# Optimization experiments

Measured on AMD Instinct MI355X. Metric: run time of the kernel, lower is better.

Reference implementation:

```python
import jax, jax.numpy as jnp
import numpy as np

HIDDEN = 128; HEADS = 8; HD = HIDDEN // HEADS; NRBF = 50; NLAYERS = 6
CUT = 5.0; MAXZ = 100
N = 5000; E = 100000


def cosine_cutoff(d):
    # cutoff_lower = 0: 0.5*(cos(pi*d/cut)+1) * (d < cut)
    return 0.5 * (jnp.cos(d * (jnp.pi / CUT)) + 1.0) * (d < CUT)


def expnorm_rbf(d, means, betas):
    # ExpNormalSmearing with cutoff_lower=0, alpha = 5/cutoff
    alpha = 5.0 / CUT
    return cosine_cutoff(d)[:, None] * jnp.exp(-betas * (jnp.exp(-alpha * d)[:, None] - means) ** 2)


def layernorm(x, w, b):
    m = x.mean(-1, keepdims=True)
    v = ((x - m) ** 2).mean(-1, keepdims=True)
    return (x - m) / jnp.sqrt(v + 1e-5) * w + b


def setup_inputs():
    key = jax.random.key(0)
    ks = jax.random.split(key, 16)
    start = float(np.exp(-CUT))

    def lin(k, fi, fo):
        return jax.random.normal(k, (fi, fo), jnp.float32) / np.sqrt(fi)

    def lin_l(k, fi, fo):
        return jax.random.normal(k, (NLAYERS, fi, fo), jnp.float32) / np.sqrt(fi)

    return {
        "z": jax.random.randint(ks[0], (N,), 0, MAXZ),
        "edge_index": jax.random.randint(ks[1], (2, E), 0, N),
        "edge_vec": jax.random.normal(ks[2], (E, 3), jnp.float32) * 1.7,
        "emb": jax.random.normal(ks[3], (MAXZ, HIDDEN), jnp.float32),
        "means": jnp.linspace(start, 1.0, NRBF, dtype=jnp.float32),
        "betas": jnp.full((NRBF,), (2.0 / NRBF * (1.0 - start)) ** -2, dtype=jnp.float32),
        "ne_emb": jax.random.normal(ks[4], (MAXZ, HIDDEN), jnp.float32),
        "dpW": lin(ks[5], NRBF, HIDDEN), "dpb": jnp.zeros((HIDDEN,), jnp.float32),
        "cbW": lin(ks[6], 2 * HIDDEN, HIDDEN), "cbb": jnp.zeros((HIDDEN,), jnp.float32),
        "lnw": jnp.ones((NLAYERS, HIDDEN), jnp.float32), "lnb": jnp.zeros((NLAYERS, HIDDEN), jnp.float32),
        "qW": lin_l(ks[7], HIDDEN, HIDDEN), "qb": jnp.zeros((NLAYERS, HIDDEN), jnp.float32),
        "kW": lin_l(ks[8], HIDDEN, HIDDEN), "kb": jnp.zeros((NLAYERS, HIDDEN), jnp.float32),
        "vW": lin_l(ks[9], HIDDEN, 3 * HIDDEN), "vb": jnp.zeros((NLAYERS, 3 * HIDDEN), jnp.float32),
        "oW": lin_l(ks[10], HIDDEN, 3 * HIDDEN), "ob": jnp.zeros((NLAYERS, 3 * HIDDEN), jnp.float32),
        "vecW": lin_l(ks[11], HIDDEN, 3 * HIDDEN),
        "dkW": lin_l(ks[12], NRBF, HIDDEN), "dkb": jnp.zeros((NLAYERS, HIDDEN), jnp.float32),
        "dvW": lin_l(ks[13], NRBF, 3 * HIDDEN), "dvb": jnp.zeros((NLAYERS, 3 * HIDDEN), jnp.float32),
        "onw": jnp.ones((HIDDEN,), jnp.float32), "onb": jnp.zeros((HIDDEN,), jnp.float32),
    }


def _forward(z, edge_index, edge_vec, emb, means, betas, ne_emb, dpW, dpb, cbW, cbb,
             lnw, lnb, qW, qb, kW, kb, vW, vb, oW, ob, vecW, dkW, dkb, dvW, dvb, onw, onb):
    src, dst = edge_index[0], edge_index[1]          # j (source), i (target)
    n = z.shape[0]
    x = emb[z]                                        # [N, H]
    ew = jnp.linalg.norm(edge_vec, axis=1)            # [E]
    ea = expnorm_rbf(ew, means, betas)                # [E, NRBF]
    nonself = src != dst
    # normalize edge vectors except self-loop edges (kept as-is, matching the torch clone/mask)
    evn = edge_vec / jnp.where(nonself, ew, 1.0)[:, None]
    cut_e = cosine_cutoff(ew)                         # [E]

    # --- NeighborEmbedding: self-loops removed from aggregation ---
    W = (ea @ dpW + dpb) * cut_e[:, None]
    W = jnp.where(nonself[:, None], W, 0.0)
    agg = jax.ops.segment_sum(ne_emb[z][src] * W, dst, num_segments=n)
    x = jnp.concatenate([x, agg], axis=1) @ cbW + cbb
    vec = jnp.zeros((n, 3, HIDDEN), x.dtype)

    def layer(carry, p):
        x, vec = carry
        h = layernorm(x, p["lnw"], p["lnb"])
        q = (h @ p["qW"] + p["qb"]).reshape(n, HEADS, HD)
        k = (h @ p["kW"] + p["kb"]).reshape(n, HEADS, HD)
        v = (h @ p["vW"] + p["vb"]).reshape(n, HEADS, 3 * HD)
        vec1, vec2, vec3 = jnp.split(jnp.einsum("nch,hk->nck", vec, p["vecW"]), 3, axis=-1)
        vec_dot = (vec1 * vec2).sum(axis=1)                    # [N, H]
        vec_h = vec.reshape(n, 3, HEADS, HD)
        dk = jax.nn.silu(ea @ p["dkW"] + p["dkb"]).reshape(-1, HEADS, HD)
        dv = jax.nn.silu(ea @ p["dvW"] + p["dvb"]).reshape(-1, HEADS, 3 * HD)
        # per-edge attention weight, silu activation, smoothly cut off
        attn = jax.nn.silu((q[dst] * k[src] * dk).sum(-1)) * cut_e[:, None]   # [E, heads]
        xm, w1, w2 = jnp.split(v[src] * dv, 3, axis=2)                        # each [E, heads, HD]
        xm = xm * attn[:, :, None]
        vecm = vec_h[src] * w1[:, None] + w2[:, None] * evn[:, :, None, None] # [E, 3, heads, HD]
        xa = jax.ops.segment_sum(xm, dst, num_segments=n).reshape(n, HIDDEN)
        va = jax.ops.segment_sum(vecm, dst, num_segments=n).reshape(n, 3, HIDDEN)
        o1, o2, o3 = jnp.split(xa @ p["oW"] + p["ob"], 3, axis=-1)
        dx = vec_dot * o2 + o3
        dvec = vec3 * o1[:, None, :] + va
        return (x + dx, vec + dvec), None

    stacked = {"lnw": lnw, "lnb": lnb, "qW": qW, "qb": qb, "kW": kW, "kb": kb,
               "vW": vW, "vb": vb, "oW": oW, "ob": ob, "vecW": vecW,
               "dkW": dkW, "dkb": dkb, "dvW": dvW, "dvb": dvb}
    (x, vec), _ = jax.lax.scan(layer, (x, vec), stacked)
    x = layernorm(x, onw, onb)
    return x, vec


def reference(z, edge_index, edge_vec, emb, means, betas, ne_emb, dpW, dpb, cbW, cbb,
              lnw, lnb, qW, qb, kW, kb, vW, vb, oW, ob, vecW, dkW, dkb, dvW, dvb, onw, onb):
    return _forward(z, edge_index, edge_vec, emb, means, betas, ne_emb, dpW, dpb, cbW, cbb,
                    lnw, lnb, qW, qb, kW, kb, vW, vb, oW, ob, vecW, dkW, dkb, dvW, dvb, onw, onb)
```

## Files before the change

### kernel.cpp

```cpp
#include <hip/hip_runtime.h>
#include <math.h>

#define HID 128
#define NRBF 50
#define NLAYERS 6
#define CUTV 5.0f
#define KNOTS 1024
#define TSCALE 204.8f
#define TINV   0.0048828125f
#define TROWS  (KNOTS + 1)
#define TRWORDS 512
#define TSTRIDE ((size_t)TROWS * TRWORDS)
#define WCOLS 1408
#define KB 16

typedef unsigned int  uint32;
typedef unsigned short ushort16;
typedef __attribute__((ext_vector_type(8))) short short8;
typedef __attribute__((ext_vector_type(4))) float f32x4;

__device__ __forceinline__ float siluf(float x){ return x / (1.0f + __expf(-x)); }
__device__ __forceinline__ float lerpf(float a, float b, float f){ return fmaf(f, b - a, a); }
__device__ __forceinline__ ushort16 f2b(float x){
    uint32 u = __float_as_uint(x);
    u += 0x7fffu + ((u >> 16) & 1u);
    return (ushort16)(u >> 16);
}
__device__ __forceinline__ float b2f(ushort16 u){ return __uint_as_float(((uint32)u) << 16); }
__device__ __forceinline__ uint32 packp(float a, float b){
    return (uint32)f2b(a) | ((uint32)f2b(b) << 16);
}
__device__ __forceinline__ float plo(uint32 u){ return __uint_as_float(u << 16); }
__device__ __forceinline__ float phi(uint32 u){ return __uint_as_float(u & 0xffff0000u); }
__device__ __forceinline__ float plerp(uint32 u, float f){ float a = plo(u); return fmaf(f, phi(u) - a, a); }

__global__ void k_zero(int* p, int n){
    int i = blockIdx.x*blockDim.x + threadIdx.x;
    if (i < n) p[i] = 0;
}

__global__ void k_count(const int* ei, int E, int* counts){
    int e = blockIdx.x*blockDim.x + threadIdx.x;
    if (e < E) atomicAdd(&counts[ei[E + e]], 1);
}

__global__ void k_scan(const int* counts, int* offsets, int* cursor, int n){
    __shared__ int part[1024];
    int tid = threadIdx.x;
    int PER = (n + 1023) >> 10;
    int base = tid * PER;
    int loc[8]; int s = 0;
    #pragma unroll 8
    for (int ii = 0; ii < 8; ii++){
        if (ii < PER){
            int idx = base + ii;
            int c = (idx < n) ? counts[idx] : 0;
            loc[ii] = s; s += c;
        }
    }
    part[tid] = s;
    __syncthreads();
    for (int off = 1; off < 1024; off <<= 1){
        int v = (tid >= off) ? part[tid - off] : 0;
        __syncthreads();
        part[tid] += v;
        __syncthreads();
    }
    int excl = (tid == 0) ? 0 : part[tid - 1];
    #pragma unroll 8
    for (int ii = 0; ii < 8; ii++){
        if (ii < PER){
            int idx = base + ii;
            if (idx < n){ int o = excl + loc[ii]; offsets[idx] = o; cursor[idx] = o; }
        }
    }
    if (tid == 1023) offsets[n] = part[1023];
}

__global__ void k_scatter(const int* ei, int E, int* cursor, int* eperm){
    int e = blockIdx.x*blockDim.x + threadIdx.x;
    if (e < E){
        int d = ei[E + e];
        int pos = atomicAdd(&cursor[d], 1);
        eperm[pos] = e;
    }
}

__global__ __launch_bounds__(256) void k_srcsort(const int* offsets, const int* ei, int* eperm, int N){
    int node = blockIdx.x*4 + (threadIdx.x >> 6);
    int lane = threadIdx.x & 63;
    if (node >= N) return;
    int r0 = offsets[node], r1 = offsets[node+1];
    for (int c0 = r0; c0 < r1; c0 += 64){
        int n = min(64, r1 - c0);
        int e = 0; int key = 0x7fffffff;
        if (lane < n){ e = eperm[c0 + lane]; key = ei[e]; }
        int rank = 0;
        for (int t = 0; t < n; t++){
            int kt = __shfl(key, t, 64);
            if (t != lane && ((kt < key) || (kt == key && t < lane))) rank++;
        }
        if (lane < n) eperm[c0 + rank] = e;
    }
}

__global__ void k_edge_vals(const int* ei, const float* edge_vec, const int* eperm, int E,
                            int4* edata, float4* evn4){
    int row = blockIdx.x*blockDim.x + threadIdx.x;
    if (row >= E) return;
    int e = eperm[row];
    int s = ei[e], d = ei[E + e];
    float vx = edge_vec[e*3+0], vy = edge_vec[e*3+1], vz = edge_vec[e*3+2];
    float ew = sqrtf(vx*vx + vy*vy + vz*vz);
    float cut = (ew < CUTV) ? 0.5f*(__cosf(ew * 0.62831853071795864f) + 1.0f) : 0.0f;
    int ns = (s != d) ? 1 : 0;
    float inv = ns ? (1.0f/ew) : 1.0f;
    float un = fminf(ew * TSCALE, (float)KNOTS);
    int j = (int)un;
    float f = un - (float)j;
    int4 ed; ed.x = s; ed.y = j; ed.z = __float_as_int(f); ed.w = __float_as_int(cut);
    edata[row] = ed;
    float4 ev; ev.x = vx*inv; ev.y = vy*inv; ev.z = vz*inv; ev.w = ns ? 1.0f : 0.0f;
    evn4[row] = ev;
}

__global__ void k_pad(ushort16* hb16, ushort16* vecm, ushort16* xab16, int N, int Nup, int N3up){
    int i = blockIdx.x*blockDim.x + threadIdx.x;
    int hpad = (Nup - N)*HID;
    int vpad = (N3up - 3*N)*HID;
    if (i < hpad){ hb16[(size_t)N*HID + i] = 0; xab16[(size_t)N*HID + i] = 0; }
    if (i < vpad) vecm[(size_t)3*N*HID + i] = 0;
}

__global__ __launch_bounds__(512) void k_build_tables(
    const float* means, const float* betas,
    const float* dkW, const float* dkb, const float* dvW, const float* dvb,
    uint32* Tp){
    int jb = blockIdx.x * KB;
    int l  = blockIdx.y;
    int c  = threadIdx.x;
    __shared__ float ea_s[KB+1][NRBF+2];
    for (int idx = c; idx < (KB+1)*NRBF; idx += 512){
        int kk = idx / NRBF, r = idx - kk*NRBF;
        float d = (jb + kk) * TINV;
        float cut = (d < CUTV) ? 0.5f*(__cosf(d * 0.62831853071795864f) + 1.0f) : 0.0f;
        float u = __expf(-d) - means[r];
        ea_s[kk][r] = cut * __expf(-betas[r]*u*u);
    }
    __syncthreads();
    int h = c >> 2, i = c & 3;
    const float* Wcol; int stride; float bias;
    if (i == 0){
        Wcol = dkW + (size_t)l*NRBF*HID + h; stride = HID;
        bias = dkb[(size_t)l*HID + h];
    } else {
        int col = ((h >> 4)*48 + (h & 15)) + 16*(i-1);
        Wcol = dvW + (size_t)l*NRBF*384 + col; stride = 384;
        bias = dvb[(size_t)l*384 + col];
    }
    float a[KB+1];
    #pragma unroll
    for (int k = 0; k <= KB; k++) a[k] = bias;
    for (int r = 0; r < NRBF; r++){
        float w = Wcol[(size_t)r*stride];
        #pragma unroll
        for (int k = 0; k <= KB; k++) a[k] += ea_s[k][r]*w;
    }
    uint32* dst = Tp + (size_t)l*TSTRIDE + (size_t)jb*TRWORDS + c;
    float sp = siluf(a[0]);
    #pragma unroll
    for (int k = 0; k < KB; k++){
        int j = jb + k;
        if (j >= TROWS) break;
        float sn = siluf(a[k+1]);
        dst[(size_t)k*TRWORDS] = packp(sp, sn);
        sp = sn;
    }
}

__global__ __launch_bounds__(128) void k_build_ne(
    const float* means, const float* betas,
    const float* dpW, const float* dpb, float2* Tne){
    int j = blockIdx.x, c = threadIdx.x;
    __shared__ float ea0[NRBF], ea1[NRBF];
    float d0 = j * TINV, d1 = (j+1) * TINV;
    float c0 = (d0 < CUTV) ? 0.5f*(__cosf(d0 * 0.62831853071795864f) + 1.0f) : 0.0f;
    float c1 = (d1 < CUTV) ? 0.5f*(__cosf(d1 * 0.62831853071795864f) + 1.0f) : 0.0f;
    if (c < NRBF){
        float m = means[c], be = betas[c];
        float u0 = __expf(-d0) - m, u1 = __expf(-d1) - m;
        ea0[c] = c0 * __expf(-be*u0*u0);
        ea1[c] = c1 * __expf(-be*u1*u1);
    }
    __syncthreads();
    float a0 = dpb[c], a1 = a0;
    #pragma unroll
    for (int r = 0; r < NRBF; r++){ float w = dpW[r*HID + c]; a0 += ea0[r]*w; a1 += ea1[r]*w; }
    float2 o; o.x = a0*c0; o.y = a1*c1;
    Tne[(size_t)j*HID + c] = o;
}

__global__ __launch_bounds__(256) void k_build_wt(
    const float* qW, const float* kW, const float* vW, const float* vecW, const float* oW,
    ushort16* WT){
    int l = blockIdx.y; int c0 = blockIdx.x*32;
    const float* W; int C; int cs;
    if (c0 < 128)      { W = qW   + (size_t)l*HID*128; C = 128; cs = c0; }
    else if (c0 < 256) { W = kW   + (size_t)l*HID*128; C = 128; cs = c0-128; }
    else if (c0 < 640) { W = vW   + (size_t)l*HID*384; C = 384; cs = c0-256; }
    else if (c0 < 1024){ W = vecW + (size_t)l*HID*384; C = 384; cs = c0-640; }
    else               { W = oW   + (size_t)l*HID*384; C = 384; cs = c0-1024; }
    __shared__ ushort16 t[128][33];
    for (int i = threadIdx.x; i < 128*32; i += 256){
        int k = i >> 5, c = i & 31;
        t[k][c] = f2b(W[(size_t)k*C + cs + c]);
    }
    __syncthreads();
    ushort16* dst = WT + (size_t)l*WCOLS*HID + (size_t)c0*HID;
    for (int i = threadIdx.x; i < 128*32; i += 256){
        int c = i >> 7, k = i & 127;
        dst[(size_t)c*HID + k] = t[k][c];
    }
}

__global__ __launch_bounds__(256) void k_mfma01(
    const ushort16* __restrict__ hb16, const ushort16* __restrict__ vecm,
    const ushort16* __restrict__ WT,
    const float* __restrict__ qbias, const float* __restrict__ kbias, const float* __restrict__ vbias,
    float* __restrict__ qo, ushort16* __restrict__ vpack,
    ushort16* __restrict__ vecout, int N){
    int cg = blockIdx.x;
    int rblk = blockIdx.y*64;
    const ushort16* A; int R; int cblk; const ushort16* wt;
    if (cg < 10){ A = hb16; R = N;   cblk = cg*64;      wt = WT; }
    else        { A = vecm; R = 3*N; cblk = (cg-10)*64; wt = WT + (size_t)640*HID; }
    if (rblk >= R) return;
    int wave = threadIdx.x >> 6, lane = threadIdx.x & 63;
    int r0 = rblk + wave*16;
    int l16 = lane & 15, lg = lane >> 4;
    short8 a[4];
    const ushort16* ar = A + (size_t)(r0 + l16)*HID + lg*8;
    #pragma unroll
    for (int ks = 0; ks < 4; ks++) a[ks] = *(const short8*)(ar + ks*32);
    f32x4 acc[4];
    #pragma unroll
    for (int ct = 0; ct < 4; ct++){ acc[ct][0]=0.f; acc[ct][1]=0.f; acc[ct][2]=0.f; acc[ct][3]=0.f; }
    #pragma unroll
    for (int ct = 0; ct < 4; ct++){
        const ushort16* br = wt + (size_t)(cblk + ct*16 + l16)*HID + lg*8;
        #pragma unroll
        for (int ks = 0; ks < 4; ks++){
            short8 b = *(const short8*)(br + ks*32);
            acc[ct] = __builtin_amdgcn_mfma_f32_16x16x32_bf16(a[ks], b, acc[ct], 0, 0, 0);
        }
    }
    #pragma unroll
    for (int ct = 0; ct < 4; ct++){
        int gc = cblk + ct*16 + l16;
        int slot = 0; float bb = 0.f; int kind;
        if (cg < 10){
            if (gc < 128){ kind = 0; bb = qbias[gc]; }
            else if (gc < 256){ kind = 1; int ck = gc - 128; slot = ck*4 + 3; bb = kbias[ck]; }
            else { kind = 2; int cv = gc - 256; int vh = (cv/48)*16 + (cv%48)%16; int vi = (cv%48)/16;
                   slot = vh*4 + vi; bb = vbias[cv]; }
        } else kind = 3;
        #pragma unroll
        for (int rg = 0; rg < 4; rg++){
            int row = r0 + lg*4 + rg;
            if (row >= R) continue;
            float v = acc[ct][rg] + bb;
            if (kind == 0)      qo[(size_t)row*HID + gc] = v;
            else if (kind == 3) vecout[(size_t)row*384 + gc] = f2b(v);
            else                vpack[(size_t)row*512 + slot] = f2b(v);
        }
    }
}

__global__ __launch_bounds__(128) void k_ne_agg(
    const int* offsets, const int4* edata, const float4* evn4, const float2* Tne,
    const int* z, const float* ne_emb, float* agg){
    int i = blockIdx.x, h = threadIdx.x;
    float acc = 0.f;
    int r0 = offsets[i], r1 = offsets[i+1];
    #pragma unroll 4
    for (int row = r0; row < r1; row++){
        int4 ed = edata[row];
        int s = ed.x, j = ed.y;
        float f = __int_as_float(ed.z);
        float mask = evn4[row].w;
        float2 tv = Tne[(size_t)j*HID + h];
        float w = lerpf(tv.x, tv.y, f) * mask;
        acc += w * ne_emb[(size_t)z[s]*HID + h];
    }
    agg[(size_t)i*HID + h] = acc;
}

__global__ __launch_bounds__(128) void k_combine_ln(
    const int* z, const float* emb, const float* agg, const float* cbW, const float* cbb,
    const float* lnw0, const float* lnb0,
    float* x, ushort16* hb16, float* vec, ushort16* vecm, uint32* vecpack, int N){
    int n0 = blockIdx.x*8, h = threadIdx.x;
    __shared__ float in_s[8][2*HID];
    int nr = min(8, N - n0);
    for (int m = 0; m < nr; m++){
        in_s[m][h]       = emb[(size_t)z[n0+m]*HID + h];
        in_s[m][HID + h] = agg[(size_t)(n0+m)*HID + h];
    }
    __syncthreads();
    float acc[8];
    #pragma unroll
    for (int m = 0; m < 8; m++) acc[m] = 0.f;
    for (int kk = 0; kk < 2*HID; kk += 4){
        float w0 = cbW[(kk+0)*HID + h], w1 = cbW[(kk+1)*HID + h];
        float w2 = cbW[(kk+2)*HID + h], w3 = cbW[(kk+3)*HID + h];
        #pragma unroll
        for (int m = 0; m < 8; m++){
            const float* a = &in_s[m][kk];
            acc[m] += a[0]*w0 + a[1]*w1 + a[2]*w2 + a[3]*w3;
        }
    }
    float bias = cbb[h], w = lnw0[h], bb = lnb0[h];
    __shared__ float r1_[2], r2_[2];
    int wid = h >> 6;
    for (int m = 0; m < nr; m++){
        int n = n0 + m;
        float v = acc[m] + bias;
        x[(size_t)n*HID + h] = v;
        float s1 = v, s2 = v*v;
        #pragma unroll
        for (int o = 32; o; o >>= 1){ s1 += __shfl_xor(s1, o, 64); s2 += __shfl_xor(s2, o, 64); }
        if ((h & 63) == 0){ r1_[wid] = s1; r2_[wid] = s2; }
        __syncthreads();
        float sum = r1_[0] + r1_[1], sumsq = r2_[0] + r2_[1];
        float mean = sum * (1.f/HID);
        float var = sumsq * (1.f/HID) - mean*mean;
        float inv = rsqrtf(var + 1e-5f);
        hb16[(size_t)n*HID + h] = f2b((v - mean)*inv*w + bb);
        __syncthreads();
        vec [(size_t)n*384 + h]       = 0.f;
        vec [(size_t)n*384 + 128 + h] = 0.f;
        vec [(size_t)n*384 + 256 + h] = 0.f;
        vecm[(size_t)n*384 + h]       = 0;
        vecm[(size_t)n*384 + 128 + h] = 0;
        vecm[(size_t)n*384 + 256 + h] = 0;
        vecpack[(size_t)n*256 + 2*h]     = 0;
        vecpack[(size_t)n*256 + 2*h + 1] = 0;
    }
}

__global__ __launch_bounds__(128) void k_edge_agg(
    const int* __restrict__ offsets, const int4* __restrict__ edata,
    const float4* __restrict__ evn4, const uint32* __restrict__ Tp,
    const float* __restrict__ q, const ushort16* __restrict__ vpack,
    const uint32* __restrict__ vecpack,
    ushort16* __restrict__ xa16, float* __restrict__ va){
    int i = blockIdx.x, h = threadIdx.x;
    float qv = q[(size_t)i*HID + h];
    float axa = 0.f, av0 = 0.f, av1 = 0.f, av2 = 0.f;
    int r0 = offsets[i], r1 = offsets[i+1];
    for (int t0 = r0; t0 < r1; t0 += 4){
        float f_[4], cut_[4], ex_[4], ey_[4], ez_[4];
        uint4 t4_[4];
        uint2 vp_[4], vc_[4];
        #pragma unroll
        for (int u = 0; u < 4; u++){
            int row = min(t0 + u, r1 - 1);
            int4 ed = edata[row];
            int s = ed.x, j = ed.y;
            f_[u]   = __int_as_float(ed.z);
            cut_[u] = __int_as_float(ed.w);
            t4_[u] = *(const uint4*)(Tp + (size_t)j*TRWORDS + 4*h);
            vp_[u] = *(const uint2*)(vpack + (size_t)s*512 + 4*h);
            vc_[u] = *(const uint2*)(vecpack + (size_t)s*256 + 2*h);
            float4 ev = evn4[row];
            ex_[u] = ev.x; ey_[u] = ev.y; ez_[u] = ev.z;
        }
        #pragma unroll
        for (int u = 0; u < 4; u++){
            if (t0 + u >= r1) break;
            float f = f_[u];
            float dk = plerp(t4_[u].x, f);
            float kv = phi(vp_[u].y);
            float p = qv * kv * dk;
            p += __shfl_xor(p, 1, 64);
            p += __shfl_xor(p, 2, 64);
            p += __shfl_xor(p, 4, 64);
            p += __shfl_xor(p, 8, 64);
            float attn = siluf(p) * cut_[u];
            float dv0 = plerp(t4_[u].y, f);
            float dv1 = plerp(t4_[u].z, f);
            float dv2 = plerp(t4_[u].w, f);
            axa += plo(vp_[u].x) * dv0 * attn;
            float w1v = phi(vp_[u].x) * dv1;
            float w2v = plo(vp_[u].y) * dv2;
            av0 += plo(vc_[u].x)*w1v + w2v*ex_[u];
            av1 += phi(vc_[u].x)*w1v + w2v*ey_[u];
            av2 += plo(vc_[u].y)*w1v + w2v*ez_[u];
        }
    }
    xa16[(size_t)i*HID + h] = f2b(axa);
    va[(size_t)i*384 + h]       = av0;
    va[(size_t)i*384 + 128 + h] = av1;
    va[(size_t)i*384 + 256 + h] = av2;
}

#define OROWS 32
__global__ __launch_bounds__(256) void k_oupd(
    const ushort16* __restrict__ xab16, const ushort16* __restrict__ WT,
    const float* __restrict__ obias,
    float* __restrict__ x, float* __restrict__ vec, ushort16* __restrict__ vecm,
    uint32* __restrict__ vecpack,
    const ushort16* __restrict__ vecout, const float* __restrict__ va,
    const float* __restrict__ lnw_n, const float* __restrict__ lnb_n,
    ushort16* __restrict__ hb16, float* __restrict__ outx, float* __restrict__ outv,
    int N, int fin){
    __shared__ float o_s[OROWS][385];
    int tile = blockIdx.x; int r0 = tile*OROWS;
    int wid = threadIdx.x >> 6, lane = threadIdx.x & 63;
    int l16 = lane & 15, lg = lane >> 4;
    {
        int rr = r0 + (wid & 1)*16;
        const ushort16* ar = xab16 + (size_t)(rr + l16)*HID + lg*8;
        short8 a[4];
        #pragma unroll
        for (int ks = 0; ks < 4; ks++) a[ks] = *(const short8*)(ar + ks*32);
        int cbase = (wid >> 1)*192;
        const ushort16* wt = WT + (size_t)1024*HID;
        #pragma unroll
        for (int ct = 0; ct < 12; ct++){
            f32x4 acc; acc[0]=0.f; acc[1]=0.f; acc[2]=0.f; acc[3]=0.f;
            const ushort16* br = wt + (size_t)(cbase + ct*16 + l16)*HID + lg*8;
            #pragma unroll
            for (int ks = 0; ks < 4; ks++){
                short8 b = *(const short8*)(br + ks*32);
                acc = __builtin_amdgcn_mfma_f32_16x16x32_bf16(a[ks], b, acc, 0, 0, 0);
            }
            int gc = cbase + ct*16 + l16;
            float bb = obias[gc];
            #pragma unroll
            for (int rg = 0; rg < 4; rg++)
                o_s[(wid & 1)*16 + lg*4 + rg][gc] = acc[rg] + bb;
        }
    }
    __syncthreads();
    for (int pass = 0; pass < 8; pass++){
        int nrow = pass*4 + wid;
        int n = r0 + nrow;
        if (n >= N) break;
        const ushort16* vo = vecout + (size_t)n*1152;
        const float* o_r = o_s[nrow];
        size_t vb = (size_t)n*384;
        float xva, xvb, v0a, v0b, v1a, v1b, v2a, v2b;
        #pragma unroll
        for (int half = 0; half < 2; half++){
            int hh = lane + half*64;
            float vdot = b2f(vo[hh])*b2f(vo[128+hh]) + b2f(vo[384+hh])*b2f(vo[512+hh])
                       + b2f(vo[768+hh])*b2f(vo[896+hh]);
            float o1 = o_r[hh], o2 = o_r[128+hh], o3 = o_r[256+hh];
            float xv = x[(size_t)n*HID + hh] + vdot*o2 + o3;
            float v0 = vec[vb + hh]       + b2f(vo[256  + hh])*o1 + va[vb + hh];
            float v1 = vec[vb + 128 + hh] + b2f(vo[640  + hh])*o1 + va[vb + 128 + hh];
            float v2 = vec[vb + 256 + hh] + b2f(vo[1024 + hh])*o1 + va[vb + 256 + hh];
            if (half == 0){ xva = xv; v0a = v0; v1a = v1; v2a = v2; }
            else          { xvb = xv; v0b = v0; v1b = v1; v2b = v2; }
        }
        float s1 = xva + xvb, s2 = xva*xva + xvb*xvb;
        #pragma unroll
        for (int o = 32; o; o >>= 1){ s1 += __shfl_xor(s1, o, 64); s2 += __shfl_xor(s2, o, 64); }
        float mean = s1 * (1.f/HID);
        float var = s2 * (1.f/HID) - mean*mean;
        float inv = rsqrtf(var + 1e-5f);
        #pragma unroll
        for (int half = 0; half < 2; half++){
            int hh = lane + half*64;
            float xv = half ? xvb : xva;
            float v0 = half ? v0b : v0a;
            float v1 = half ? v1b : v1a;
            float v2 = half ? v2b : v2a;
            float lnv = (xv - mean)*inv*lnw_n[hh] + lnb_n[hh];
            if (!fin){
                x[(size_t)n*HID + hh] = xv;
                vec[vb + hh] = v0; vec[vb + 128 + hh] = v1; vec[vb + 256 + hh] = v2;
                vecm[vb + hh] = f2b(v0); vecm[vb + 128 + hh] = f2b(v1); vecm[vb + 256 + hh] = f2b(v2);
                vecpack[(size_t)n*256 + 2*hh]     = packp(v0, v1);
                vecpack[(size_t)n*256 + 2*hh + 1] = packp(v2, 0.f);
                hb16[(size_t)n*HID + hh] = f2b(lnv);
            } else {
                outx[(size_t)n*HID + hh] = lnv;
                outv[vb + hh] = v0; outv[vb + 128 + hh] = v1; outv[vb + 256 + hh] = v2;
            }
        }
    }
}

extern "C" void kernel_launch(void* const* d_in, const int* in_sizes, int n_in,
                              void* d_out, int out_size, void* d_ws, size_t ws_size,
                              hipStream_t stream){
    const int*   z        = (const int*)  d_in[0];
    const int*   ei       = (const int*)  d_in[1];
    const float* edge_vec = (const float*)d_in[2];
    const float* emb      = (const float*)d_in[3];
    const float* means    = (const float*)d_in[4];
    const float* betas    = (const float*)d_in[5];
    const float* ne_emb   = (const float*)d_in[6];
    const float* dpW      = (const float*)d_in[7];
    const float* dpb      = (const float*)d_in[8];
    const float* cbW      = (const float*)d_in[9];
    const float* cbb      = (const float*)d_in[10];
    const float* lnw      = (const float*)d_in[11];
    const float* lnb      = (const float*)d_in[12];
    const float* qW       = (const float*)d_in[13];
    const float* qb       = (const float*)d_in[14];
    const float* kW       = (const float*)d_in[15];
    const float* kb       = (const float*)d_in[16];
    const float* vW       = (const float*)d_in[17];
    const float* vb       = (const float*)d_in[18];
    const float* oW       = (const float*)d_in[19];
    const float* obias    = (const float*)d_in[20];
    const float* vecW     = (const float*)d_in[21];
    const float* dkW      = (const float*)d_in[22];
    const float* dkb      = (const float*)d_in[23];
    const float* dvW      = (const float*)d_in[24];
    const float* dvb      = (const float*)d_in[25];
    const float* onw      = (const float*)d_in[26];
    const float* onb      = (const float*)d_in[27];

    int N = in_sizes[0];
    int E = in_sizes[1] / 2;
    int Nup  = ((N + 63) >> 6) << 6;
    int N3up = ((3*N + 63) >> 6) << 6;

    char* p = (char*)d_ws;
    auto alloc = [&](size_t bytes){ void* r = (void*)p; p += (bytes + 255) & ~(size_t)255; return r; };
    int*      counts  = (int*)     alloc((size_t)N*4);
    int*      offsets = (int*)     alloc((size_t)(N+1)*4);
    int*      cursor  = (int*)     alloc((size_t)N*4);
    int*      eperm   = (int*)     alloc((size_t)E*4);
    int4*     edata   = (int4*)    alloc((size_t)E*16);
    float4*   evn4    = (float4*)  alloc((size_t)E*16);
    uint32*   Tp      = (uint32*)  alloc((size_t)NLAYERS*TSTRIDE*4);
    float2*   Tne     = (float2*)  alloc((size_t)TROWS*HID*8);
    ushort16* WT      = (ushort16*)alloc((size_t)NLAYERS*WCOLS*HID*2);
    float*    agg     = (float*)   alloc((size_t)N*HID*4);
    float*    xb      = (float*)   alloc((size_t)N*HID*4);
    ushort16* hb16    = (ushort16*)alloc((size_t)Nup*HID*2);
    float*    qb_     = (float*)   alloc((size_t)N*HID*4);
    ushort16* vpack   = (ushort16*)alloc((size_t)N*512*2);
    uint32*   vecpack = (uint32*)  alloc((size_t)N*256*4);
    ushort16* vecm    = (ushort16*)alloc((size_t)N3up*HID*2);
    float*    vecb    = (float*)   alloc((size_t)N*384*4);
    ushort16* vecout  = (ushort16*)alloc((size_t)N*1152*2);
    ushort16* xab16   = (ushort16*)alloc((size_t)Nup*HID*2);
    float*    vab     = (float*)   alloc((size_t)N*384*4);

    k_zero<<<(N+255)/256, 256, 0, stream>>>(counts, N);
    k_count<<<(E+255)/256, 256, 0, stream>>>(ei, E, counts);
    k_scan<<<1, 1024, 0, stream>>>(counts, offsets, cursor, N);
    k_scatter<<<(E+255)/256, 256, 0, stream>>>(ei, E, cursor, eperm);
    k_srcsort<<<(N+3)/4, 256, 0, stream>>>(offsets, ei, eperm, N);
    k_edge_vals<<<(E+255)/256, 256, 0, stream>>>(ei, edge_vec, eperm, E, edata, evn4);
    k_pad<<<((Nup-N)*HID + (N3up-3*N)*HID + 255)/256 + 1, 256, 0, stream>>>(hb16, vecm, xab16, N, Nup, N3up);

    k_build_tables<<<dim3((TROWS + KB - 1)/KB, NLAYERS), 512, 0, stream>>>(means, betas, dkW, dkb, dvW, dvb, Tp);
    k_build_ne<<<TROWS, 128, 0, stream>>>(means, betas, dpW, dpb, Tne);
    k_build_wt<<<dim3(WCOLS/32, NLAYERS), 256, 0, stream>>>(qW, kW, vW, vecW, oW, WT);
    k_ne_agg<<<N, 128, 0, stream>>>(offsets, edata, evn4, Tne, z, ne_emb, agg);
    k_combine_ln<<<(N+7)/8, 128, 0, stream>>>(z, emb, agg, cbW, cbb, lnw, lnb,
                                              xb, hb16, vecb, vecm, vecpack, N);

    float* outx = (float*)d_out;
    float* outv = (float*)d_out + (size_t)N*HID;

    for (int l = 0; l < NLAYERS; l++){
        const ushort16* WTl = WT + (size_t)l*WCOLS*HID;
        k_mfma01<<<dim3(16, (3*N+63)/64), 256, 0, stream>>>(hb16, vecm, WTl,
            qb + (size_t)l*HID, kb + (size_t)l*HID, vb + (size_t)l*384,
            qb_, vpack, vecout, N);
        k_edge_agg<<<N, 128, 0, stream>>>(offsets, edata, evn4, Tp + (size_t)l*TSTRIDE,
                                          qb_, vpack, vecpack, xab16, vab);
        int fin = (l == NLAYERS-1);
        k_oupd<<<(N + OROWS - 1)/OROWS, 256, 0, stream>>>(xab16, WTl, obias + (size_t)l*384,
            xb, vecb, vecm, vecpack, vecout, vab,
            fin ? onw : lnw + (size_t)(l+1)*HID,
            fin ? onb : lnb + (size_t)(l+1)*HID,
            hb16, outx, outv, N, fin);
    }
}
```

Before: 704.3 us.

## Pre-permute K/V weight columns into packed order and stage GEMM output through LDS

The K and V weight columns (and their biases) are reordered at build time to match the interleaved vpack slot layout, so the projection kernel writes contiguous columns instead of scattered 2-byte stores. Output tiles for vpack and vecout are staged in shared memory and written back as coalesced 32-bit row segments. This targets uncoalesced global stores in the per-layer projection kernel. It adds an LDS round trip, a block barrier and a small bias-build kernel.

```diff
diff --git a/kernel.cpp b/kernel.cpp
--- a/kernel.cpp
+++ b/kernel.cpp
@@ -204,16 +204,20 @@
     const float* qW, const float* kW, const float* vW, const float* vecW, const float* oW,
     ushort16* WT){
     int l = blockIdx.y; int c0 = blockIdx.x*32;
-    const float* W; int C; int cs;
-    if (c0 < 128)      { W = qW   + (size_t)l*HID*128; C = 128; cs = c0; }
-    else if (c0 < 256) { W = kW   + (size_t)l*HID*128; C = 128; cs = c0-128; }
-    else if (c0 < 640) { W = vW   + (size_t)l*HID*384; C = 384; cs = c0-256; }
-    else if (c0 < 1024){ W = vecW + (size_t)l*HID*384; C = 384; cs = c0-640; }
-    else               { W = oW   + (size_t)l*HID*384; C = 384; cs = c0-1024; }
     __shared__ ushort16 t[128][33];
     for (int i = threadIdx.x; i < 128*32; i += 256){
         int k = i >> 5, c = i & 31;
-        t[k][c] = f2b(W[(size_t)k*C + cs + c]);
+        int gcol = c0 + c;
+        const float* W; int C; int oc;
+        if (gcol < 128)      { W = qW   + (size_t)l*HID*128; C = 128; oc = gcol; }
+        else if (gcol < 640) {
+            int s = gcol - 128; int h = s >> 2, si = s & 3;
+            if (si == 3){ W = kW + (size_t)l*HID*128; C = 128; oc = h; }
+            else        { W = vW + (size_t)l*HID*384; C = 384; oc = (h>>4)*48 + (h&15) + 16*si; }
+        }
+        else if (gcol < 1024){ W = vecW + (size_t)l*HID*384; C = 384; oc = gcol-640; }
+        else                 { W = oW   + (size_t)l*HID*384; C = 384; oc = gcol-1024; }
+        t[k][c] = f2b(W[(size_t)k*C + oc]);
     }
     __syncthreads();
     ushort16* dst = WT + (size_t)l*WCOLS*HID + (size_t)c0*HID;
@@ -223,10 +227,19 @@
     }
 }
 
+__global__ __launch_bounds__(512) void k_build_bias(
+    const float* kb, const float* vb, float* kvbias){
+    int l = blockIdx.x, s = threadIdx.x;
+    int h = s >> 2, i = s & 3;
+    float v = (i == 3) ? kb[(size_t)l*HID + h]
+                       : vb[(size_t)l*384 + (h>>4)*48 + (h&15) + 16*i];
+    kvbias[(size_t)l*512 + s] = v;
+}
+
 __global__ __launch_bounds__(256) void k_mfma01(
     const ushort16* __restrict__ hb16, const ushort16* __restrict__ vecm,
-    const ushort16* __restrict__ WT,
-    const float* __restrict__ qbias, const float* __restrict__ kbias, const float* __restrict__ vbias,
+    const ushort16* __restrict__ WT, const float* __restrict__ qbias,
+    const float* __restrict__ kvbias,
     float* __restrict__ qo, ushort16* __restrict__ vpack,
     ushort16* __restrict__ vecout, int N){
     int cg = blockIdx.x;
@@ -254,24 +267,42 @@
             acc[ct] = __builtin_amdgcn_mfma_f32_16x16x32_bf16(a[ks], b, acc[ct], 0, 0, 0);
         }
     }
+    __shared__ ushort16 lds[64][72];
+    if (cg < 2){
+        #pragma unroll
+        for (int ct = 0; ct < 4; ct++){
+            int gc = cblk + ct*16 + l16;
+            float bb = qbias[gc];
+            #pragma unroll
+            for (int rg = 0; rg < 4; rg++){
+                int row = r0 + lg*4 + rg;
+                if (row < R) qo[(size_t)row*HID + gc] = acc[ct][rg] + bb;
+            }
+        }
+        return;
+    }
+    const float* bias = (cg < 10) ? (kvbias + (cblk - 128)) : nullptr;
     #pragma unroll
     for (int ct = 0; ct < 4; ct++){
-        int gc = cblk + ct*16 + l16;
-        int slot = 0; float bb = 0.f; int kind;
-        if (cg < 10){
-            if (gc < 128){ kind = 0; bb = qbias[gc]; }
-            else if (gc < 256){ kind = 1; int ck = gc - 128; slot = ck*4 + 3; bb = kbias[ck]; }
-            else { kind = 2; int cv = gc - 256; int vh = (cv/48)*16 + (cv%48)%16; int vi = (cv%48)/16;
-                   slot = vh*4 + vi; bb = vbias[cv]; }
-        } else kind = 3;
-        #pragma unroll
-        for (int rg = 0; rg < 4; rg++){
-            int row = r0 + lg*4 + rg;
-            if (row >= R) continue;
-            float v = acc[ct][rg] + bb;
-            if (kind == 0)      qo[(size_t)row*HID + gc] = v;
-            else if (kind == 3) vecout[(size_t)row*384 + gc] = f2b(v);
-            else                vpack[(size_t)row*512 + slot] = f2b(v);
+        int lc = ct*16 + l16;
+        float bb = bias ? bias[lc] : 0.f;
+        #pragma unroll
+        for (int rg = 0; rg < 4; rg++)
+            lds[wave*16 + lg*4 + rg][lc] = f2b(acc[ct][rg] + bb);
+    }
+    __syncthreads();
+    ushort16* out; int stride, colbase;
+    if (cg < 10){ out = vpack;  stride = 512; colbase = cblk - 128; }
+    else        { out = vecout; stride = 384; colbase = cblk; }
+    const uint32* l32 = (const uint32*)&lds[0][0];
+    #pragma unroll
+    for (int it = 0; it < 8; it++){
+        int idx = it*256 + threadIdx.x;
+        int row = idx >> 5, cp = idx & 31;
+        int grow = rblk + row;
+        if (grow < R){
+            uint32 val = l32[row*36 + cp];
+            *((uint32*)(out + (size_t)grow*stride + colbase) + cp) = val;
         }
     }
 }
@@ -541,6 +572,7 @@
     uint32*   Tp      = (uint32*)  alloc((size_t)NLAYERS*TSTRIDE*4);
     float2*   Tne     = (float2*)  alloc((size_t)TROWS*HID*8);
     ushort16* WT      = (ushort16*)alloc((size_t)NLAYERS*WCOLS*HID*2);
+    float*    kvbias  = (float*)   alloc((size_t)NLAYERS*512*4);
     float*    agg     = (float*)   alloc((size_t)N*HID*4);
     float*    xb      = (float*)   alloc((size_t)N*HID*4);
     ushort16* hb16    = (ushort16*)alloc((size_t)Nup*HID*2);
@@ -564,6 +596,7 @@
     k_build_tables<<<dim3((TROWS + KB - 1)/KB, NLAYERS), 512, 0, stream>>>(means, betas, dkW, dkb, dvW, dvb, Tp);
     k_build_ne<<<TROWS, 128, 0, stream>>>(means, betas, dpW, dpb, Tne);
     k_build_wt<<<dim3(WCOLS/32, NLAYERS), 256, 0, stream>>>(qW, kW, vW, vecW, oW, WT);
+    k_build_bias<<<NLAYERS, 512, 0, stream>>>(kb, vb, kvbias);
     k_ne_agg<<<N, 128, 0, stream>>>(offsets, edata, evn4, Tne, z, ne_emb, agg);
     k_combine_ln<<<(N+7)/8, 128, 0, stream>>>(z, emb, agg, cbW, cbb, lnw, lnb,
                                               xb, hb16, vecb, vecm, vecpack, N);
@@ -574,7 +607,7 @@
     for (int l = 0; l < NLAYERS; l++){
         const ushort16* WTl = WT + (size_t)l*WCOLS*HID;
         k_mfma01<<<dim3(16, (3*N+63)/64), 256, 0, stream>>>(hb16, vecm, WTl,
-            qb + (size_t)l*HID, kb + (size_t)l*HID, vb + (size_t)l*384,
+            qb + (size_t)l*HID, kvbias + (size_t)l*512,
             qb_, vpack, vecout, N);
         k_edge_agg<<<N, 128, 0, stream>>>(offsets, edata, evn4, Tp + (size_t)l*TSTRIDE,
                                           qb_, vpack, vecpack, xab16, vab);
```

New measurement: 670.4 us. 1.05x faster.
